# Kernel optimization log

Measured on AMD Instinct MI355X. Metric: run time of the kernel, lower is better.

Reference implementation:

```python
import jax, jax.numpy as jnp
import numpy as np

N_NODES = 50000

def gcn_conv(x, src, dst, W, b, n_nodes):
    # PyG GCNConv: add self-loops, symmetric deg^{-1/2} normalization,
    # linear transform, scatter-add aggregation (source -> target), bias.
    loop = jnp.arange(n_nodes, dtype=src.dtype)
    src2 = jnp.concatenate([src, loop])
    dst2 = jnp.concatenate([dst, loop])
    deg = jax.ops.segment_sum(jnp.ones_like(dst2, dtype=x.dtype), dst2, num_segments=n_nodes)
    dinv = jnp.where(deg > 0, jax.lax.rsqrt(deg), 0.0)
    norm = dinv[src2] * dinv[dst2]  # [E + N]
    h = x @ W                        # [N, out]
    msg = h[src2] * norm[:, None]    # gather + scale
    out = jax.ops.segment_sum(msg, dst2, num_segments=n_nodes)
    return out + b

def setup_inputs() -> dict:
    key = jax.random.key(0)
    k1, k2, k3, k4 = jax.random.split(key, 4)
    x = jax.random.normal(k1, (N_NODES, 64), dtype=jnp.float32)
    edge_index = jax.random.randint(k2, (2, 800000), 0, N_NODES, dtype=jnp.int64)
    # Glorot-ish init for weights
    W1 = jax.random.normal(k3, (64, 128), dtype=jnp.float32) * (1.0 / np.sqrt(64))
    b1 = jnp.zeros((128,), dtype=jnp.float32)
    W2 = jax.random.normal(k4, (128, 8), dtype=jnp.float32) * (1.0 / np.sqrt(128))
    b2 = jnp.zeros((8,), dtype=jnp.float32)
    return {"x": x, "edge_index": edge_index, "W1": W1, "b1": b1, "W2": W2, "b2": b2}

def reference(x, edge_index, W1, b1, W2, b2):
    src, dst = edge_index[0], edge_index[1]
    h = gcn_conv(x, src, dst, W1, b1, N_NODES)
    h = jax.nn.relu(h)
    out = gcn_conv(h, src, dst, W2, b2, N_NODES)
    return out
```

## Files before the change

kernel.cpp:

```cpp
#include <hip/hip_runtime.h>

#define IN1 64
#define MID 128
#define OUT2 8
#define YPAD 136
#define TPAD 68
#define CAP 64

__device__ __forceinline__ unsigned short f2bf(float f) {
    unsigned int u = __float_as_uint(f);
    unsigned int r = (u + 0x7fff + ((u >> 16) & 1)) >> 16;
    return (unsigned short)r;
}
__device__ __forceinline__ float bflo(unsigned int u) { return __uint_as_float(u << 16); }
__device__ __forceinline__ float bfhi(unsigned int u) { return __uint_as_float(u & 0xffff0000u); }

__global__ __launch_bounds__(256) void k_fill(const int* __restrict__ src,
                                              const int* __restrict__ dst,
                                              int* __restrict__ cnt,
                                              unsigned short* __restrict__ col,
                                              const float4* __restrict__ x4,
                                              ushort4* __restrict__ xb4,
                                              int E4, int E, int npx, int slices, int n16) {
    for (int gid = blockIdx.x * 256 + (int)threadIdx.x; gid < n16; gid += gridDim.x * 256) {
        float4 vx = x4[gid];
        ushort4 pv;
        pv.x = f2bf(vx.x); pv.y = f2bf(vx.y);
        pv.z = f2bf(vx.z); pv.w = f2bf(vx.w);
        xb4[gid] = pv;
    }

    int xcd = blockIdx.x & 7;
    int slice = blockIdx.x >> 3;
    int lo = xcd * npx, hi = lo + npx;
    int eps = (E4 + slices - 1) / slices;
    int g0 = slice * eps, g1 = min(E4, g0 + eps);
    int g = g0 + (int)threadIdx.x;
    if (g < g1) {
        int4 dv = ((const int4*)dst)[g];
        int4 sv = ((const int4*)src)[g];
        for (;;) {
            int gn = g + 256;
            bool has = gn < g1;
            int4 dn, sn;
            if (has) { dn = ((const int4*)dst)[gn]; sn = ((const int4*)src)[gn]; }
            if (dv.x >= lo && dv.x < hi) {
                int p = atomicAdd(&cnt[dv.x], 1);
                if (p < CAP) col[dv.x * CAP + p] = (unsigned short)sv.x;
            }
            if (dv.y >= lo && dv.y < hi) {
                int p = atomicAdd(&cnt[dv.y], 1);
                if (p < CAP) col[dv.y * CAP + p] = (unsigned short)sv.y;
            }
            if (dv.z >= lo && dv.z < hi) {
                int p = atomicAdd(&cnt[dv.z], 1);
                if (p < CAP) col[dv.z * CAP + p] = (unsigned short)sv.z;
            }
            if (dv.w >= lo && dv.w < hi) {
                int p = atomicAdd(&cnt[dv.w], 1);
                if (p < CAP) col[dv.w * CAP + p] = (unsigned short)sv.w;
            }
            if (!has) break;
            dv = dn; sv = sn;
            g = gn;
        }
    }
    if (blockIdx.x == 0 && threadIdx.x == 0) {
        for (int e = E4 * 4; e < E; ++e) {
            int d = dst[e];
            int p = atomicAdd(&cnt[d], 1);
            if (p < CAP) col[d * CAP + p] = (unsigned short)src[e];
        }
    }
}

__global__ __launch_bounds__(256) void k_node(const uint4* __restrict__ xb4,
                                              const int* __restrict__ cnt,
                                              const unsigned short* __restrict__ col,
                                              const float* __restrict__ W1,
                                              const float* __restrict__ b1,
                                              const float* __restrict__ W2,
                                              float* __restrict__ z, int n) {
    __shared__ float w2s[MID * OUT2];
    __shared__ float tS[4][8][TPAD];
    __shared__ float yS[4][8][YPAD];

    int t = threadIdx.x;
    ((float4*)w2s)[t] = ((const float4*)W2)[t];

    int lane = t & 63, wave = t >> 6;
    int g = lane >> 3;
    int fl = lane & 7;
    int row0 = blockIdx.x * 32 + wave * 8;
    int row = row0 + g;
    bool valid = row < n;

    float a0=0.f,a1=0.f,a2=0.f,a3=0.f,a4=0.f,a5=0.f,a6=0.f,a7=0.f;
    int deg = 0, base = 0;
    if (valid) {
        int c0 = cnt[row];
        deg = min(c0, CAP);
        base = row * CAP;
        float dself = rsqrtf((float)(c0 + 1));
        uint4 u = xb4[(size_t)row * 8 + fl];
        a0 = dself * bflo(u.x); a1 = dself * bfhi(u.x);
        a2 = dself * bflo(u.y); a3 = dself * bfhi(u.y);
        a4 = dself * bflo(u.z); a5 = dself * bfhi(u.z);
        a6 = dself * bflo(u.w); a7 = dself * bfhi(u.w);
    }
    int cv = (deg >= 8) ? col[base + fl] : 0;
    int j = 0;
    for (; j + 8 <= deg; j += 8) {
        int cvn = (j + 16 <= deg) ? col[base + j + 8 + fl] : 0;
#pragma unroll
        for (int p = 0; p < 8; ++p) {
            int s = __shfl(cv, (g << 3) + p, 64);
            int cs = cnt[s];
            uint4 u = xb4[(size_t)s * 8 + fl];
            float ds = rsqrtf((float)(cs + 1));
            a0 = fmaf(ds, bflo(u.x), a0); a1 = fmaf(ds, bfhi(u.x), a1);
            a2 = fmaf(ds, bflo(u.y), a2); a3 = fmaf(ds, bfhi(u.y), a3);
            a4 = fmaf(ds, bflo(u.z), a4); a5 = fmaf(ds, bfhi(u.z), a5);
            a6 = fmaf(ds, bflo(u.w), a6); a7 = fmaf(ds, bfhi(u.w), a7);
        }
        cv = cvn;
    }
    int rem = deg - j;
    if (rem > 0) {
        int cvr = col[base + min(j + fl, CAP - 1)];
#pragma unroll
        for (int p = 0; p < 8; ++p) {
            if (p < rem) {
                int s = __shfl(cvr, (g << 3) + p, 64);
                int cs = cnt[s];
                uint4 u = xb4[(size_t)s * 8 + fl];
                float ds = rsqrtf((float)(cs + 1));
                a0 = fmaf(ds, bflo(u.x), a0); a1 = fmaf(ds, bfhi(u.x), a1);
                a2 = fmaf(ds, bflo(u.y), a2); a3 = fmaf(ds, bfhi(u.y), a3);
                a4 = fmaf(ds, bflo(u.z), a4); a5 = fmaf(ds, bfhi(u.z), a5);
                a6 = fmaf(ds, bflo(u.w), a6); a7 = fmaf(ds, bfhi(u.w), a7);
            }
        }
    }
    {
        float4 w0 = {a0, a1, a2, a3};
        float4 w1v = {a4, a5, a6, a7};
        *(float4*)&tS[wave][g][8 * fl] = w0;
        *(float4*)&tS[wave][g][8 * fl + 4] = w1v;
    }

    float dnd[8];
#pragma unroll
    for (int k = 0; k < 8; ++k) {
        int ck = cnt[min(row0 + k, n - 1)];
        dnd[k] = rsqrtf((float)(ck + 1));
    }

    float ya[8], yb[8];
#pragma unroll
    for (int i = 0; i < 8; ++i) { ya[i] = 0.f; yb[i] = 0.f; }
#pragma unroll 2
    for (int k4 = 0; k4 < IN1; k4 += 4) {
        float4 tv[8];
#pragma unroll
        for (int nd = 0; nd < 8; ++nd) tv[nd] = *(const float4*)&tS[wave][nd][k4];
#pragma unroll
        for (int kk = 0; kk < 4; ++kk) {
            int k = k4 + kk;
            float wa = W1[k * MID + lane];
            float wb = W1[k * MID + lane + 64];
#pragma unroll
            for (int nd = 0; nd < 8; ++nd) {
                float e = (&tv[nd].x)[kk];
                ya[nd] = fmaf(e, wa, ya[nd]);
                yb[nd] = fmaf(e, wb, yb[nd]);
            }
        }
    }
    float bl = b1[lane], bh = b1[lane + 64];
#pragma unroll
    for (int nd = 0; nd < 8; ++nd) {
        yS[wave][nd][lane] = fmaxf(fmaf(ya[nd], dnd[nd], bl), 0.f);
        yS[wave][nd][lane + 64] = fmaxf(fmaf(yb[nd], dnd[nd], bh), 0.f);
    }

    __syncthreads();

    int nd2 = lane >> 3, ch = lane & 7;
    float p[OUT2];
#pragma unroll
    for (int c = 0; c < OUT2; ++c) p[c] = 0.0f;
#pragma unroll
    for (int kk = 0; kk < 16; ++kk) {
        int k = kk * 8 + ch;
        float yk = yS[wave][nd2][k];
        float4 wlo = *(const float4*)&w2s[k * OUT2];
        float4 whi = *(const float4*)&w2s[k * OUT2 + 4];
        p[0] = fmaf(yk, wlo.x, p[0]); p[1] = fmaf(yk, wlo.y, p[1]);
        p[2] = fmaf(yk, wlo.z, p[2]); p[3] = fmaf(yk, wlo.w, p[3]);
        p[4] = fmaf(yk, whi.x, p[4]); p[5] = fmaf(yk, whi.y, p[5]);
        p[6] = fmaf(yk, whi.z, p[6]); p[7] = fmaf(yk, whi.w, p[7]);
    }
#pragma unroll
    for (int off = 1; off < 8; off <<= 1) {
#pragma unroll
        for (int c = 0; c < OUT2; ++c) p[c] += __shfl_xor(p[c], off, 64);
    }
    int rw = row0 + nd2;
    if (rw < n) {
        z[(size_t)rw * OUT2 + ch] = p[ch] * dnd[nd2];
    }
}

__global__ __launch_bounds__(256) void k_gather2(const int* __restrict__ cnt,
                                                 const unsigned short* __restrict__ col,
                                                 const float* __restrict__ z,
                                                 const float* __restrict__ b2,
                                                 float* __restrict__ out, int n) {
    int t = threadIdx.x, lane = t & 63, wave = t >> 6;
    int node = blockIdx.x * 4 + wave;
    if (node >= n) return;
    int nb = lane >> 3, c = lane & 7;
    float acc = (nb == 0) ? z[(size_t)node * OUT2 + c] : 0.0f;
    int c0 = cnt[node];
    int deg = min(c0, CAP);
    int base = node * CAP;
    int j = nb;
    if (j + 8 < deg) {
        int s0 = col[base + j], s1 = col[base + j + 8];
        for (; j + 8 < deg;) {
            int jn = j + 16;
            int t0 = 0, t1 = 0;
            bool has = jn + 8 < deg;
            if (has) { t0 = col[base + jn]; t1 = col[base + jn + 8]; }
            acc += z[(size_t)s0 * OUT2 + c] + z[(size_t)s1 * OUT2 + c];
            j = jn;
            if (!has) break;
            s0 = t0; s1 = t1;
        }
    }
    if (j < deg) acc += z[(size_t)col[base + j] * OUT2 + c];
#pragma unroll
    for (int off = 8; off < 64; off <<= 1) acc += __shfl_xor(acc, off, 64);
    if (lane < OUT2) out[(size_t)node * OUT2 + lane] = fmaf(acc, rsqrtf((float)(c0 + 1)), b2[lane]);
}

extern "C" void kernel_launch(void* const* d_in, const int* in_sizes, int n_in,
                              void* d_out, int out_size, void* d_ws, size_t ws_size,
                              hipStream_t stream) {
    const float* x  = (const float*)d_in[0];
    const int*   ei = (const int*)d_in[1];
    const float* W1 = (const float*)d_in[2];
    const float* b1 = (const float*)d_in[3];
    const float* W2 = (const float*)d_in[4];
    const float* b2 = (const float*)d_in[5];
    float* out = (float*)d_out;

    int N = in_sizes[0] / IN1;
    int E = in_sizes[1] / 2;
    const int* src = ei;
    const int* dst = ei + E;

    int* cnt = (int*)d_ws;
    unsigned short* col = (unsigned short*)(cnt + N);
    float* z = (float*)(col + (size_t)N * CAP);
    unsigned short* xb = (unsigned short*)(z + (size_t)N * OUT2);

    const int B = 256;
    int E4 = E / 4;
    int npx = (N + 7) / 8;
    int slices = 256;
    int n16 = N * 16;

    hipMemsetAsync(cnt, 0, (size_t)N * sizeof(int), stream);
    k_fill<<<slices * 8, B, 0, stream>>>(src, dst, cnt, col,
                                         (const float4*)x, (ushort4*)xb,
                                         E4, E, npx, slices, n16);
    k_node<<<(N + 31) / 32, 256, 0, stream>>>((const uint4*)xb, cnt, col, W1, b1, W2, z, N);
    k_gather2<<<(N + 3) / 4, 256, 0, stream>>>(cnt, col, z, b2, out, N);
}
```

Baseline: 165.9 us.

## Split bf16 conversion into its own kernel with cnt zeroing, precompute neighbor norms per lane

New measurement: 170.9 us. 3.0% more time.

```diff
diff --git a/kernel.cpp b/kernel.cpp
--- a/kernel.cpp
+++ b/kernel.cpp
@@ -15,21 +15,24 @@
 __device__ __forceinline__ float bflo(unsigned int u) { return __uint_as_float(u << 16); }
 __device__ __forceinline__ float bfhi(unsigned int u) { return __uint_as_float(u & 0xffff0000u); }
 
+__global__ __launch_bounds__(256) void k_xb(const float4* __restrict__ x4,
+                                            ushort4* __restrict__ xb4,
+                                            int* __restrict__ cnt, int n16, int N) {
+    int gid = blockIdx.x * 256 + (int)threadIdx.x;
+    if (gid < N) cnt[gid] = 0;
+    if (gid >= n16) return;
+    float4 vx = x4[gid];
+    ushort4 pv;
+    pv.x = f2bf(vx.x); pv.y = f2bf(vx.y);
+    pv.z = f2bf(vx.z); pv.w = f2bf(vx.w);
+    xb4[gid] = pv;
+}
+
 __global__ __launch_bounds__(256) void k_fill(const int* __restrict__ src,
                                               const int* __restrict__ dst,
                                               int* __restrict__ cnt,
                                               unsigned short* __restrict__ col,
-                                              const float4* __restrict__ x4,
-                                              ushort4* __restrict__ xb4,
-                                              int E4, int E, int npx, int slices, int n16) {
-    for (int gid = blockIdx.x * 256 + (int)threadIdx.x; gid < n16; gid += gridDim.x * 256) {
-        float4 vx = x4[gid];
-        ushort4 pv;
-        pv.x = f2bf(vx.x); pv.y = f2bf(vx.y);
-        pv.z = f2bf(vx.z); pv.w = f2bf(vx.w);
-        xb4[gid] = pv;
-    }
-
+                                              int E4, int E, int npx, int slices) {
     int xcd = blockIdx.x & 7;
     int slice = blockIdx.x >> 3;
     int lo = xcd * npx, hi = lo + npx;
@@ -109,32 +112,35 @@
         a6 = dself * bflo(u.w); a7 = dself * bfhi(u.w);
     }
     int cv = (deg >= 8) ? col[base + fl] : 0;
+    float dsv = rsqrtf((float)(cnt[cv] + 1));
     int j = 0;
     for (; j + 8 <= deg; j += 8) {
         int cvn = (j + 16 <= deg) ? col[base + j + 8 + fl] : 0;
+        float dsn = rsqrtf((float)(cnt[cvn] + 1));
 #pragma unroll
         for (int p = 0; p < 8; ++p) {
-            int s = __shfl(cv, (g << 3) + p, 64);
-            int cs = cnt[s];
+            int sl = (g << 3) + p;
+            int s = __shfl(cv, sl, 64);
+            float ds = __shfl(dsv, sl, 64);
             uint4 u = xb4[(size_t)s * 8 + fl];
-            float ds = rsqrtf((float)(cs + 1));
             a0 = fmaf(ds, bflo(u.x), a0); a1 = fmaf(ds, bfhi(u.x), a1);
             a2 = fmaf(ds, bflo(u.y), a2); a3 = fmaf(ds, bfhi(u.y), a3);
             a4 = fmaf(ds, bflo(u.z), a4); a5 = fmaf(ds, bfhi(u.z), a5);
             a6 = fmaf(ds, bflo(u.w), a6); a7 = fmaf(ds, bfhi(u.w), a7);
         }
-        cv = cvn;
+        cv = cvn; dsv = dsn;
     }
     int rem = deg - j;
     if (rem > 0) {
         int cvr = col[base + min(j + fl, CAP - 1)];
+        float dsr = rsqrtf((float)(cnt[cvr] + 1));
 #pragma unroll
         for (int p = 0; p < 8; ++p) {
             if (p < rem) {
-                int s = __shfl(cvr, (g << 3) + p, 64);
-                int cs = cnt[s];
+                int sl = (g << 3) + p;
+                int s = __shfl(cvr, sl, 64);
+                float ds = __shfl(dsr, sl, 64);
                 uint4 u = xb4[(size_t)s * 8 + fl];
-                float ds = rsqrtf((float)(cs + 1));
                 a0 = fmaf(ds, bflo(u.x), a0); a1 = fmaf(ds, bfhi(u.x), a1);
                 a2 = fmaf(ds, bflo(u.y), a2); a3 = fmaf(ds, bfhi(u.y), a3);
                 a4 = fmaf(ds, bflo(u.z), a4); a5 = fmaf(ds, bfhi(u.z), a5);
@@ -272,10 +278,8 @@
     int slices = 256;
     int n16 = N * 16;
 
-    hipMemsetAsync(cnt, 0, (size_t)N * sizeof(int), stream);
-    k_fill<<<slices * 8, B, 0, stream>>>(src, dst, cnt, col,
-                                         (const float4*)x, (ushort4*)xb,
-                                         E4, E, npx, slices, n16);
+    k_xb<<<(n16 + B - 1) / B, B, 0, stream>>>((const float4*)x, (ushort4*)xb, cnt, n16, N);
+    k_fill<<<slices * 8, B, 0, stream>>>(src, dst, cnt, col, E4, E, npx, slices);
     k_node<<<(N + 31) / 32, 256, 0, stream>>>((const uint4*)xb, cnt, col, W1, b1, W2, z, N);
     k_gather2<<<(N + 3) / 4, 256, 0, stream>>>(cnt, col, z, b2, out, N);
 }
```
